# Optimization experiments

Hardware: AMD Instinct MI355X
Metric: run time of the kernel (lower is better)

## Reference

```python
import jax, jax.numpy as jnp
import numpy as np

B, L, D = 16, 1024, 256
H, FF = 8, 2048
DH = D // H
EPS = 1e-5


def setup_inputs() -> dict:
    key = jax.random.key(0)
    ks = jax.random.split(key, 13)
    s = 0.02
    return {
        "x": jax.random.normal(ks[0], (B, L, D), jnp.float32),
        "Wq": jax.random.normal(ks[1], (D, D), jnp.float32) * s,
        "bq": jnp.zeros((D,), jnp.float32),
        "Wk": jax.random.normal(ks[2], (D, D), jnp.float32) * s,
        "bk": jnp.zeros((D,), jnp.float32),
        "Wv": jax.random.normal(ks[3], (D, D), jnp.float32) * s,
        "bv": jnp.zeros((D,), jnp.float32),
        "Wo": jax.random.normal(ks[4], (D, D), jnp.float32) * s,
        "bo": jnp.zeros((D,), jnp.float32),
        "W1": jax.random.normal(ks[5], (D, FF), jnp.float32) * s,
        "b1": jnp.zeros((FF,), jnp.float32),
        "W2": jax.random.normal(ks[6], (FF, D), jnp.float32) * s,
        "b2": jnp.zeros((D,), jnp.float32),
        "g1": jnp.ones((D,), jnp.float32),
        "be1": jnp.zeros((D,), jnp.float32),
        "g2": jnp.ones((D,), jnp.float32),
        "be2": jnp.zeros((D,), jnp.float32),
    }


def _layernorm(x, g, b):
    m = jnp.mean(x, axis=-1, keepdims=True)
    v = jnp.mean(jnp.square(x - m), axis=-1, keepdims=True)
    return (x - m) * jax.lax.rsqrt(v + EPS) * g + b


def reference(x, Wq, bq, Wk, bk, Wv, bv, Wo, bo, W1, b1, W2, b2, g1, be1, g2, be2):
    b, l, d = x.shape
    # QKV projections, split heads (torch split/cat == reshape to [b,l,H,dh])
    q = (x @ Wq + bq).reshape(b, l, H, DH)
    k = (x @ Wk + bk).reshape(b, l, H, DH)
    v = (x @ Wv + bv).reshape(b, l, H, DH)
    # scaled dot-product attention per head
    scores = jnp.einsum("bqhd,bkhd->bhqk", q, k) / np.float32(DH) ** 0.5
    attn = jax.nn.softmax(scores, axis=-1)
    o = jnp.einsum("bhqk,bkhd->bqhd", attn, v).reshape(b, l, d)
    o = o @ Wo + bo
    # residual + LN1 (dropout p=0.0 -> identity)
    h = _layernorm(x + o, g1, be1)
    # FFN + residual + LN2
    ff = jax.nn.relu(h @ W1 + b1) @ W2 + b2
    return _layernorm(h + ff, g2, be2)
```

## Files before the change

kernel.cpp:

```cpp
#include <hip/hip_runtime.h>
#include <math.h>

#define B_  16
#define L_  1024
#define D_  256
#define H_  8
#define DH_ 32
#define FF_ 2048
#define NROW (B_*L_)
#define QKVS 768

typedef __attribute__((ext_vector_type(8))) short short8;
typedef __attribute__((ext_vector_type(4))) short short4v;
typedef __attribute__((ext_vector_type(4))) float f32x4;
typedef __attribute__((ext_vector_type(4))) unsigned uint4v;
typedef __attribute__((ext_vector_type(4))) unsigned short ushort4v;
typedef unsigned short ushortT;

__device__ inline ushortT f2bf(float f) {
    unsigned u = __builtin_bit_cast(unsigned, f);
    u += 0x7fffu + ((u >> 16) & 1u);
    return (ushortT)(u >> 16);
}

__device__ inline float bf2f(ushortT u) {
    return __builtin_bit_cast(float, (unsigned)u << 16);
}

__device__ inline float fexp2(float x) {
#if __has_builtin(__builtin_amdgcn_exp2f)
    return __builtin_amdgcn_exp2f(x);
#else
    return exp2f(x);
#endif
}

__device__ inline void gload_lds16(const ushortT* g, ushortT* l) {
    __builtin_amdgcn_global_load_lds(
        (const __attribute__((address_space(1))) unsigned*)g,
        (__attribute__((address_space(3))) unsigned*)l, 16, 0, 0);
}

__device__ inline unsigned lds_addr(const void* p) {
    return (unsigned)(size_t)(const __attribute__((address_space(3))) void*)p;
}

template<bool RELU, bool OBF16>
__global__ __launch_bounds__(256)
void gemm_bf16_kernel(const ushortT* __restrict__ A, const ushortT* __restrict__ Bt,
                      const float* __restrict__ bias, void* __restrict__ Cv,
                      int K, int ldb, int ldc)
{
    __shared__ ushortT As[2][128 * 32];
    __shared__ ushortT Bs[2][128 * 32];

    const int tid   = threadIdx.x;
    const int w     = tid >> 6;
    const int lane  = tid & 63;
    const int qlane = lane & 15;
    const int g     = lane >> 4;
    const int wm    = w >> 1, wn = w & 1;
    const int m0    = (blockIdx.x & 127) * 128;
    const int n0    = (blockIdx.x >> 7) * 128;

    int srowA[2], sq[2];
    #pragma unroll
    for (int j = 0; j < 2; ++j) {
        int idx = (j * 4 + w) * 64 + lane;
        srowA[j] = idx >> 2;
        sq[j]    = idx & 3;
    }

    f32x4 acc[4][4];
    #pragma unroll
    for (int mi = 0; mi < 4; ++mi)
        #pragma unroll
        for (int ni = 0; ni < 4; ++ni)
            acc[mi][ni] = (f32x4){0.f, 0.f, 0.f, 0.f};

    auto stage = [&](int buf, int kt) {
        const int k0 = kt * 32;
        #pragma unroll
        for (int j = 0; j < 2; ++j) {
            gload_lds16(A + (size_t)(m0 + srowA[j]) * K + k0 + sq[j] * 8,
                        &As[buf][(j * 4 + w) * 512]);
            gload_lds16(Bt + (size_t)(n0 + srowA[j]) * ldb + k0 + sq[j] * 8,
                        &Bs[buf][(j * 4 + w) * 512]);
        }
    };

    stage(0, 0);
    __syncthreads();

    const int nt = K >> 5;
    for (int t = 0; t < nt; ++t) {
        const int cur = t & 1;
        if (t + 1 < nt) stage(cur ^ 1, t + 1);

        short8 af[4], bfr[4];
        #pragma unroll
        for (int mi = 0; mi < 4; ++mi)
            af[mi] = *(const short8*)&As[cur][(wm * 64 + mi * 16 + qlane) * 32 + g * 8];
        #pragma unroll
        for (int ni = 0; ni < 4; ++ni)
            bfr[ni] = *(const short8*)&Bs[cur][(wn * 64 + ni * 16 + qlane) * 32 + g * 8];

        #pragma unroll
        for (int mi = 0; mi < 4; ++mi)
            #pragma unroll
            for (int ni = 0; ni < 4; ++ni)
                acc[mi][ni] = __builtin_amdgcn_mfma_f32_16x16x32_bf16(
                    af[mi], bfr[ni], acc[mi][ni], 0, 0, 0);

        __syncthreads();
    }

    #pragma unroll
    for (int mi = 0; mi < 4; ++mi) {
        #pragma unroll
        for (int ni = 0; ni < 4; ++ni) {
            const int n = n0 + wn * 64 + ni * 16 + qlane;
            const float bval = bias ? bias[n] : 0.f;
            #pragma unroll
            for (int r = 0; r < 4; ++r) {
                const int m = m0 + wm * 64 + mi * 16 + 4 * g + r;
                float v = acc[mi][ni][r] + bval;
                if (RELU)  v = fmaxf(v, 0.f);
                if (OBF16) ((ushortT*)Cv)[(size_t)m * ldc + n] = f2bf(v);
                else       ((float*)Cv)[(size_t)m * ldc + n] = v;
            }
        }
    }
}

template<bool OBF16>
__global__ __launch_bounds__(256)
void gemm64_kernel(const ushortT* __restrict__ A, const ushortT* __restrict__ Bt,
                   const float* __restrict__ bias, void* __restrict__ Cv, int K)
{
    __shared__ ushortT As[2][64 * 32];
    __shared__ ushortT Bs[2][64 * 32];

    const int tid   = threadIdx.x;
    const int w     = tid >> 6;
    const int lane  = tid & 63;
    const int qlane = lane & 15;
    const int g     = lane >> 4;
    const int bid   = blockIdx.x;
    const int m0    = (bid & 255) * 64;
    const int n0    = (bid >> 8) * 64;

    const int srow = tid >> 2;
    const int sq   = tid & 3;

    f32x4 acc[4];
    #pragma unroll
    for (int ni = 0; ni < 4; ++ni) acc[ni] = (f32x4){0.f, 0.f, 0.f, 0.f};

    auto stage = [&](int buf, int kt) {
        const int k0 = kt * 32;
        gload_lds16(A + (size_t)(m0 + srow) * K + k0 + sq * 8, &As[buf][w * 512]);
        gload_lds16(Bt + (size_t)(n0 + srow) * K + k0 + sq * 8, &Bs[buf][w * 512]);
    };

    stage(0, 0);
    __syncthreads();

    const int nt = K >> 5;
    for (int t = 0; t < nt; ++t) {
        const int cur = t & 1;
        if (t + 1 < nt) stage(cur ^ 1, t + 1);

        short8 af = *(const short8*)&As[cur][(w * 16 + qlane) * 32 + g * 8];
        short8 bfr[4];
        #pragma unroll
        for (int ni = 0; ni < 4; ++ni)
            bfr[ni] = *(const short8*)&Bs[cur][(ni * 16 + qlane) * 32 + g * 8];

        #pragma unroll
        for (int ni = 0; ni < 4; ++ni)
            acc[ni] = __builtin_amdgcn_mfma_f32_16x16x32_bf16(af, bfr[ni], acc[ni], 0, 0, 0);

        __syncthreads();
    }

    #pragma unroll
    for (int ni = 0; ni < 4; ++ni) {
        const int n = n0 + ni * 16 + qlane;
        const float bval = bias[n];
        #pragma unroll
        for (int r = 0; r < 4; ++r) {
            const int m = m0 + w * 16 + 4 * g + r;
            float v = acc[ni][r] + bval;
            if (OBF16) ((ushortT*)Cv)[(size_t)m * D_ + n] = f2bf(v);
            else       ((float*)Cv)[(size_t)m * D_ + n] = v;
        }
    }
}

template<bool XF32, bool YF32, bool OBF16>
__global__ __launch_bounds__(256)
void ln_kernel(const void* __restrict__ X, const void* __restrict__ Y,
               const float* __restrict__ g, const float* __restrict__ bb,
               void* __restrict__ out)
{
    const int tid  = threadIdx.x;
    const int lane = tid & 63;
    const int w    = tid >> 6;
    const size_t row = (size_t)blockIdx.x * 4 + w;
    const int c    = lane * 4;

    float xv[4], yv[4];
    if (XF32) {
        float4 v = *reinterpret_cast<const float4*>((const float*)X + row * D_ + c);
        xv[0] = v.x; xv[1] = v.y; xv[2] = v.z; xv[3] = v.w;
    } else {
        ushort4v v = *reinterpret_cast<const ushort4v*>((const ushortT*)X + row * D_ + c);
        #pragma unroll
        for (int j = 0; j < 4; ++j) xv[j] = bf2f(v[j]);
    }
    if (YF32) {
        float4 v = *reinterpret_cast<const float4*>((const float*)Y + row * D_ + c);
        yv[0] = v.x; yv[1] = v.y; yv[2] = v.z; yv[3] = v.w;
    } else {
        ushort4v v = *reinterpret_cast<const ushort4v*>((const ushortT*)Y + row * D_ + c);
        #pragma unroll
        for (int j = 0; j < 4; ++j) yv[j] = bf2f(v[j]);
    }

    float s0 = xv[0] + yv[0], s1 = xv[1] + yv[1], s2 = xv[2] + yv[2], s3 = xv[3] + yv[3];

    float sum = s0 + s1 + s2 + s3;
    float sq  = s0 * s0 + s1 * s1 + s2 * s2 + s3 * s3;
    #pragma unroll
    for (int off = 1; off < 64; off <<= 1) {
        sum += __shfl_xor(sum, off);
        sq  += __shfl_xor(sq, off);
    }
    const float mean = sum * (1.f / D_);
    const float var  = sq * (1.f / D_) - mean * mean;
    const float rinv = rsqrtf(var + 1e-5f);

    const float4 gv = *reinterpret_cast<const float4*>(g + c);
    const float4 bv = *reinterpret_cast<const float4*>(bb + c);
    float o0 = (s0 - mean) * rinv * gv.x + bv.x;
    float o1 = (s1 - mean) * rinv * gv.y + bv.y;
    float o2 = (s2 - mean) * rinv * gv.z + bv.z;
    float o3 = (s3 - mean) * rinv * gv.w + bv.w;

    if (OBF16) {
        unsigned p0 = (unsigned)f2bf(o0) | ((unsigned)f2bf(o1) << 16);
        unsigned p1 = (unsigned)f2bf(o2) | ((unsigned)f2bf(o3) << 16);
        uint2 u = {p0, p1};
        *reinterpret_cast<uint2*>((ushortT*)out + row * D_ + c) = u;
    } else {
        float4 ov = {o0, o1, o2, o3};
        *reinterpret_cast<float4*>((float*)out + row * D_ + c) = ov;
    }
}

__global__ __launch_bounds__(512)
void attn_mfma_kernel(const ushortT* __restrict__ qkv, ushortT* __restrict__ o)
{
    __shared__ __align__(16) ushortT K4[2][2048];
    __shared__ __align__(16) ushortT Vs[2][2048];

    const int tid   = threadIdx.x;
    const int lane  = tid & 63;
    const int w     = tid >> 6;
    const int qlane = lane & 15;
    const int g     = lane >> 4;

    const int bid = blockIdx.x;
    const int bh  = bid & 127;
    const int b   = bh >> 3;
    const int h   = bh & 7;
    const int q0  = (bid >> 7) * 128;

    const size_t inbase = (size_t)b * L_ * QKVS + h * 32;
    const size_t obase  = (size_t)b * L_ * 256 + h * 32;

    const short8 qf = *(const short8*)(qkv + inbase + (size_t)(q0 + w * 16 + qlane) * QKVS + g * 8);

    f32x4 ot0 = {0.f, 0.f, 0.f, 0.f}, ot1 = {0.f, 0.f, 0.f, 0.f};
    float l_reg = 0.f;

    const float CEXP = 0.25503540f;

    const int t2   = tid & 255;
    const int skey = t2 >> 2;
    const int sg   = t2 & 3;
    const bool isK = tid < 256;
    const ushortT* src = qkv + inbase + (isK ? 256 : 512) + sg * 8 + (size_t)skey * QKVS;

    char* K4b = (char*)&K4[0][0];
    char* Vsb = (char*)&Vs[0][0];

    unsigned kwoff = (unsigned)sg * 1024u + (unsigned)skey * 16u;
    kwoff ^= (kwoff >> 5) & 0x60;
    const unsigned vwoff = ((unsigned)((skey >> 2) * 2 + (sg >> 1))) * 128u +
                           ((unsigned)(skey & 3)) * 32u +
                           ((((unsigned)(sg & 1)) ^ ((unsigned)(sg >> 1))) * 16u);
    char* wbase = isK ? K4b : Vsb;
    const unsigned woff = isK ? kwoff : vwoff;

    unsigned kroff[4];
    #pragma unroll
    for (int kt4 = 0; kt4 < 4; ++kt4) {
        unsigned off = (unsigned)g * 1024u + (unsigned)(kt4 * 16 + qlane) * 16u;
        kroff[kt4] = off ^ ((off >> 5) & 0x60);
    }
    const unsigned vrbase  = lds_addr(&Vs[0][0]) + 256u * (unsigned)g + 8u * (unsigned)qlane;
    const unsigned vrbase2 = vrbase ^ 64u;

    short8 reg = *(const short8*)src;

    #pragma unroll 2
    for (int t = 0; t < L_ / 64; ++t) {
        const unsigned bo = (unsigned)(t & 1) * 4096u;
        *(short8*)(wbase + bo + woff) = reg;
        if (t + 1 < L_ / 64)
            reg = *(const short8*)(src + (size_t)((t + 1) * 64) * QKVS);
        __syncthreads();

        f32x4 st[4];
        __builtin_amdgcn_s_setprio(1);
        #pragma unroll
        for (int kt4 = 0; kt4 < 4; ++kt4) {
            short8 kf = *(const short8*)(K4b + bo + kroff[kt4]);
            st[kt4] = __builtin_amdgcn_mfma_f32_16x16x32_bf16(kf, qf, (f32x4){0.f,0.f,0.f,0.f}, 0, 0, 0);
        }
        __builtin_amdgcn_s_setprio(0);

        float p[16];
        float s4[4];
        #pragma unroll
        for (int kt4 = 0; kt4 < 4; ++kt4) {
            #pragma unroll
            for (int r = 0; r < 4; ++r)
                p[kt4 * 4 + r] = fexp2(st[kt4][r] * CEXP);
            s4[kt4] = (p[kt4*4] + p[kt4*4+1]) + (p[kt4*4+2] + p[kt4*4+3]);
        }
        float ssum = (s4[0] + s4[1]) + (s4[2] + s4[3]);
        ssum += __shfl_xor(ssum, 16);
        ssum += __shfl_xor(ssum, 32);
        l_reg += ssum;

        unsigned pk_[8];
        #pragma unroll
        for (int i = 0; i < 8; ++i)
            asm("v_cvt_pk_bf16_f32 %0, %1, %2" : "=v"(pk_[i]) : "v"(p[2*i]), "v"(p[2*i+1]));
        const short8 pa0 = __builtin_bit_cast(short8, (uint4v){pk_[0], pk_[1], pk_[2], pk_[3]});
        const short8 pa1 = __builtin_bit_cast(short8, (uint4v){pk_[4], pk_[5], pk_[6], pk_[7]});

        const unsigned va  = vrbase  + bo;
        const unsigned va2 = vrbase2 + bo;
        __builtin_amdgcn_s_setprio(1);
        {
            short4v v00, v01, v10, v11;
            asm volatile("ds_read_b64_tr_b16 %0, %1"             : "=v"(v00) : "v"(va));
            asm volatile("ds_read_b64_tr_b16 %0, %1 offset:1024" : "=v"(v01) : "v"(va));
            asm volatile("ds_read_b64_tr_b16 %0, %1 offset:128"  : "=v"(v10) : "v"(va2));
            asm volatile("ds_read_b64_tr_b16 %0, %1 offset:1152" : "=v"(v11) : "v"(va2));
            asm volatile("s_waitcnt lgkmcnt(0)" ::: "memory");
            __builtin_amdgcn_sched_barrier(0);
            short8 vb0 = __builtin_shufflevector(v00, v01, 0,1,2,3,4,5,6,7);
            short8 vb1 = __builtin_shufflevector(v10, v11, 0,1,2,3,4,5,6,7);
            ot0 = __builtin_amdgcn_mfma_f32_16x16x32_bf16(pa0, vb0, ot0, 0, 0, 0);
            ot1 = __builtin_amdgcn_mfma_f32_16x16x32_bf16(pa0, vb1, ot1, 0, 0, 0);
        }
        {
            short4v v00, v01, v10, v11;
            asm volatile("ds_read_b64_tr_b16 %0, %1 offset:2048" : "=v"(v00) : "v"(va));
            asm volatile("ds_read_b64_tr_b16 %0, %1 offset:3072" : "=v"(v01) : "v"(va));
            asm volatile("ds_read_b64_tr_b16 %0, %1 offset:2176" : "=v"(v10) : "v"(va2));
            asm volatile("ds_read_b64_tr_b16 %0, %1 offset:3200" : "=v"(v11) : "v"(va2));
            asm volatile("s_waitcnt lgkmcnt(0)" ::: "memory");
            __builtin_amdgcn_sched_barrier(0);
            short8 vb0 = __builtin_shufflevector(v00, v01, 0,1,2,3,4,5,6,7);
            short8 vb1 = __builtin_shufflevector(v10, v11, 0,1,2,3,4,5,6,7);
            ot0 = __builtin_amdgcn_mfma_f32_16x16x32_bf16(pa1, vb0, ot0, 0, 0, 0);
            ot1 = __builtin_amdgcn_mfma_f32_16x16x32_bf16(pa1, vb1, ot1, 0, 0, 0);
        }
        __builtin_amdgcn_s_setprio(0);
    }

    const float linv = 1.f / l_reg;
    #pragma unroll
    for (int r = 0; r < 4; ++r) {
        float lr = __shfl(linv, 4 * g + r);
        size_t row = (size_t)(q0 + w * 16 + 4 * g + r);
        ushortT* op = o + obase + row * 256;
        op[qlane]      = f2bf(ot0[r] * lr);
        op[16 + qlane] = f2bf(ot1[r] * lr);
    }
}

__global__ __launch_bounds__(256)
void prep_kernel(const float* __restrict__ x, ushortT* __restrict__ xb,
                 const float* __restrict__ Wq, const float* __restrict__ Wk,
                 const float* __restrict__ Wv, const float* __restrict__ Wo,
                 ushortT* __restrict__ Wqkvb, ushortT* __restrict__ Wob,
                 const float* __restrict__ W1, ushortT* __restrict__ W1b,
                 const float* __restrict__ W2, ushortT* __restrict__ W2b,
                 const float* __restrict__ bq, const float* __restrict__ bk,
                 const float* __restrict__ bv, float* __restrict__ bqkv)
{
    __shared__ float t[32][33];
    const int bid = blockIdx.x;
    const int tid = threadIdx.x;

    if (bid < 4096) {
        const int i = (bid * 256 + tid) * 4;
        float4 v = *reinterpret_cast<const float4*>(x + i);
        unsigned p0 = (unsigned)f2bf(v.x) | ((unsigned)f2bf(v.y) << 16);
        unsigned p1 = (unsigned)f2bf(v.z) | ((unsigned)f2bf(v.w) << 16);
        uint2 u = {p0, p1};
        *reinterpret_cast<uint2*>(xb + i) = u;
        return;
    }
    int i = bid - 4096;
    const float* W; ushortT* Wt; int K, N, bx, by;
    if (i < 256) {
        const int which = i >> 6, j = i & 63;
        bx = j & 7; by = j >> 3; K = 256; N = 256;
        W  = which == 0 ? Wq : which == 1 ? Wk : which == 2 ? Wv : Wo;
        Wt = which == 0 ? Wqkvb : which == 1 ? Wqkvb + 65536
           : which == 2 ? Wqkvb + 131072 : Wob;
    } else if (i < 768) {
        const int j = i - 256; bx = j & 63; by = j >> 6; K = 256; N = 2048;
        W = W1; Wt = W1b;
    } else if (i < 1280) {
        const int j = i - 768; bx = j & 7; by = j >> 3; K = 2048; N = 256;
        W = W2; Wt = W2b;
    } else {
        for (int k = tid; k < 768; k += 256)
            bqkv[k] = k < 256 ? bq[k] : (k < 512 ? bk[k - 256] : bv[k - 512]);
        return;
    }
    const int tx = tid & 31, ty = tid >> 5;
    const int k0 = by * 32, n0 = bx * 32;
    #pragma unroll
    for (int r = ty; r < 32; r += 8) t[r][tx] = W[(size_t)(k0 + r) * N + n0 + tx];
    __syncthreads();
    #pragma unroll
    for (int r = ty; r < 32; r += 8) Wt[(size_t)(n0 + r) * K + k0 + tx] = f2bf(t[tx][r]);
}

extern "C" void kernel_launch(void* const* d_in, const int* in_sizes, int n_in,
                              void* d_out, int out_size, void* d_ws, size_t ws_size,
                              hipStream_t stream)
{
    const float* x   = (const float*)d_in[0];
    const float* Wq  = (const float*)d_in[1];
    const float* bq  = (const float*)d_in[2];
    const float* Wk  = (const float*)d_in[3];
    const float* bk  = (const float*)d_in[4];
    const float* Wv  = (const float*)d_in[5];
    const float* bv  = (const float*)d_in[6];
    const float* Wo  = (const float*)d_in[7];
    const float* bo  = (const float*)d_in[8];
    const float* W1  = (const float*)d_in[9];
    const float* b1  = (const float*)d_in[10];
    const float* W2  = (const float*)d_in[11];
    const float* b2  = (const float*)d_in[12];
    const float* g1  = (const float*)d_in[13];
    const float* be1 = (const float*)d_in[14];
    const float* g2  = (const float*)d_in[15];
    const float* be2 = (const float*)d_in[16];
    float* out = (float*)d_out;

    char* wsb = (char*)d_ws;
    const size_t MB = (size_t)1 << 20;
    ushortT* Wqkvb = (ushortT*)(wsb);
    ushortT* Wob   = (ushortT*)(wsb + 393216);
    ushortT* W1b   = (ushortT*)(wsb + 512 * 1024);
    ushortT* W2b   = (ushortT*)(wsb + 1536 * 1024);
    float*   bqkv  = (float*)  (wsb + 2560 * 1024);
    ushortT* xb  = (ushortT*)(wsb + 3 * MB);
    ushortT* qkv = (ushortT*)(wsb + 11 * MB);
    ushortT* ob  = (ushortT*)(wsb + 35 * MB);
    ushortT* ao  = (ushortT*)(wsb + 43 * MB);
    ushortT* hb  = (ushortT*)(wsb + 3 * MB);
    ushortT* f1  = (ushortT*)(wsb + 11 * MB);

    prep_kernel<<<dim3(5377), dim3(256), 0, stream>>>(
        x, xb, Wq, Wk, Wv, Wo, Wqkvb, Wob, W1, W1b, W2, W2b, bq, bk, bv, bqkv);

    gemm_bf16_kernel<false, true><<<dim3(768), dim3(256), 0, stream>>>(
        xb, Wqkvb, bqkv, qkv, 256, 256, QKVS);

    attn_mfma_kernel<<<dim3(1024), dim3(512), 0, stream>>>(qkv, ob);

    gemm64_kernel<true><<<dim3(1024), dim3(256), 0, stream>>>(ob, Wob, bo, ao, 256);

    ln_kernel<false, false, true><<<dim3(NROW / 4), dim3(256), 0, stream>>>(
        xb, ao, g1, be1, hb);

    gemm_bf16_kernel<true, true><<<dim3(2048), dim3(256), 0, stream>>>(
        hb, W1b, b1, f1, 256, 256, FF_);

    gemm64_kernel<false><<<dim3(1024), dim3(256), 0, stream>>>(f1, W2b, b2, out, 2048);

    ln_kernel<false, true, false><<<dim3(NROW / 4), dim3(256), 0, stream>>>(
        hb, out, g2, be2, out);
}
```

Before: 145.3 us.

## Swizzle GEMM LDS tiles, deepen K-step to 64, unroll attention by two tiles

Applies an XOR swizzle to the LDS layout of both GEMM kernels to avoid bank conflicts. The 64x64 GEMM now stages K in steps of 64 instead of 32, which halves the number of barriers, and it gains RELU and ldc parameters so it can replace the 128x128 kernel for the W1 FFN GEMM (8192 blocks). The attention kernel loads two 64-key tiles per barrier using larger double buffers. The trade-offs are more LDS per block and smaller tiles for the FFN1 GEMM, which lowers operand reuse.

```diff
diff --git a/kernel.cpp b/kernel.cpp
--- a/kernel.cpp
+++ b/kernel.cpp
@@ -68,8 +68,9 @@
     for (int j = 0; j < 2; ++j) {
         int idx = (j * 4 + w) * 64 + lane;
         srowA[j] = idx >> 2;
-        sq[j]    = idx & 3;
-    }
+        sq[j]    = (idx & 3) ^ (srowA[j] & 3);
+    }
+    const int rsw = (g ^ (qlane & 3)) * 8;
 
     f32x4 acc[4][4];
     #pragma unroll
@@ -100,10 +101,10 @@
         short8 af[4], bfr[4];
         #pragma unroll
         for (int mi = 0; mi < 4; ++mi)
-            af[mi] = *(const short8*)&As[cur][(wm * 64 + mi * 16 + qlane) * 32 + g * 8];
+            af[mi] = *(const short8*)&As[cur][(wm * 64 + mi * 16 + qlane) * 32 + rsw];
         #pragma unroll
         for (int ni = 0; ni < 4; ++ni)
-            bfr[ni] = *(const short8*)&Bs[cur][(wn * 64 + ni * 16 + qlane) * 32 + g * 8];
+            bfr[ni] = *(const short8*)&Bs[cur][(wn * 64 + ni * 16 + qlane) * 32 + rsw];
 
         #pragma unroll
         for (int mi = 0; mi < 4; ++mi)
@@ -133,13 +134,14 @@
     }
 }
 
-template<bool OBF16>
+template<bool RELU, bool OBF16>
 __global__ __launch_bounds__(256)
 void gemm64_kernel(const ushortT* __restrict__ A, const ushortT* __restrict__ Bt,
-                   const float* __restrict__ bias, void* __restrict__ Cv, int K)
+                   const float* __restrict__ bias, void* __restrict__ Cv,
+                   int K, int ldc)
 {
-    __shared__ ushortT As[2][64 * 32];
-    __shared__ ushortT Bs[2][64 * 32];
+    __shared__ ushortT As[2][64 * 64];
+    __shared__ ushortT Bs[2][64 * 64];
 
     const int tid   = threadIdx.x;
     const int w     = tid >> 6;
@@ -150,36 +152,50 @@
     const int m0    = (bid & 255) * 64;
     const int n0    = (bid >> 8) * 64;
 
-    const int srow = tid >> 2;
-    const int sq   = tid & 3;
+    int srow[2], sq[2];
+    #pragma unroll
+    for (int j = 0; j < 2; ++j) {
+        const int c = j * 256 + tid;
+        srow[j] = c >> 3;
+        sq[j]   = (c & 7) ^ (srow[j] & 7);
+    }
 
     f32x4 acc[4];
     #pragma unroll
     for (int ni = 0; ni < 4; ++ni) acc[ni] = (f32x4){0.f, 0.f, 0.f, 0.f};
 
     auto stage = [&](int buf, int kt) {
-        const int k0 = kt * 32;
-        gload_lds16(A + (size_t)(m0 + srow) * K + k0 + sq * 8, &As[buf][w * 512]);
-        gload_lds16(Bt + (size_t)(n0 + srow) * K + k0 + sq * 8, &Bs[buf][w * 512]);
+        const int k0 = kt * 64;
+        #pragma unroll
+        for (int j = 0; j < 2; ++j) {
+            gload_lds16(A + (size_t)(m0 + srow[j]) * K + k0 + sq[j] * 8,
+                        &As[buf][(j * 256 + tid) * 8]);
+            gload_lds16(Bt + (size_t)(n0 + srow[j]) * K + k0 + sq[j] * 8,
+                        &Bs[buf][(j * 256 + tid) * 8]);
+        }
     };
 
     stage(0, 0);
     __syncthreads();
 
-    const int nt = K >> 5;
+    const int arow = w * 16 + qlane;
+    const int nt = K >> 6;
     for (int t = 0; t < nt; ++t) {
         const int cur = t & 1;
         if (t + 1 < nt) stage(cur ^ 1, t + 1);
 
-        short8 af = *(const short8*)&As[cur][(w * 16 + qlane) * 32 + g * 8];
-        short8 bfr[4];
-        #pragma unroll
-        for (int ni = 0; ni < 4; ++ni)
-            bfr[ni] = *(const short8*)&Bs[cur][(ni * 16 + qlane) * 32 + g * 8];
-
-        #pragma unroll
-        for (int ni = 0; ni < 4; ++ni)
-            acc[ni] = __builtin_amdgcn_mfma_f32_16x16x32_bf16(af, bfr[ni], acc[ni], 0, 0, 0);
+        #pragma unroll
+        for (int ks = 0; ks < 2; ++ks) {
+            const int aq = (ks * 4 + g) ^ (arow & 7);
+            short8 af = *(const short8*)&As[cur][arow * 64 + aq * 8];
+            #pragma unroll
+            for (int ni = 0; ni < 4; ++ni) {
+                const int brow = ni * 16 + qlane;
+                const int bq = (ks * 4 + g) ^ (brow & 7);
+                short8 bfr = *(const short8*)&Bs[cur][brow * 64 + bq * 8];
+                acc[ni] = __builtin_amdgcn_mfma_f32_16x16x32_bf16(af, bfr, acc[ni], 0, 0, 0);
+            }
+        }
 
         __syncthreads();
     }
@@ -192,8 +208,9 @@
         for (int r = 0; r < 4; ++r) {
             const int m = m0 + w * 16 + 4 * g + r;
             float v = acc[ni][r] + bval;
-            if (OBF16) ((ushortT*)Cv)[(size_t)m * D_ + n] = f2bf(v);
-            else       ((float*)Cv)[(size_t)m * D_ + n] = v;
+            if (RELU)  v = fmaxf(v, 0.f);
+            if (OBF16) ((ushortT*)Cv)[(size_t)m * ldc + n] = f2bf(v);
+            else       ((float*)Cv)[(size_t)m * ldc + n] = v;
         }
     }
 }
@@ -262,8 +279,8 @@
 __global__ __launch_bounds__(512)
 void attn_mfma_kernel(const ushortT* __restrict__ qkv, ushortT* __restrict__ o)
 {
-    __shared__ __align__(16) ushortT K4[2][2048];
-    __shared__ __align__(16) ushortT Vs[2][2048];
+    __shared__ __align__(16) ushortT K4[2][2][2048];
+    __shared__ __align__(16) ushortT Vs[2][2][2048];
 
     const int tid   = threadIdx.x;
     const int lane  = tid & 63;
@@ -293,8 +310,8 @@
     const bool isK = tid < 256;
     const ushortT* src = qkv + inbase + (isK ? 256 : 512) + sg * 8 + (size_t)skey * QKVS;
 
-    char* K4b = (char*)&K4[0][0];
-    char* Vsb = (char*)&Vs[0][0];
+    char* K4b = (char*)&K4[0][0][0];
+    char* Vsb = (char*)&Vs[0][0][0];
 
     unsigned kwoff = (unsigned)sg * 1024u + (unsigned)skey * 16u;
     kwoff ^= (kwoff >> 5) & 0x60;
@@ -310,79 +327,88 @@
         unsigned off = (unsigned)g * 1024u + (unsigned)(kt4 * 16 + qlane) * 16u;
         kroff[kt4] = off ^ ((off >> 5) & 0x60);
     }
-    const unsigned vrbase  = lds_addr(&Vs[0][0]) + 256u * (unsigned)g + 8u * (unsigned)qlane;
+    const unsigned vrbase  = lds_addr(&Vs[0][0][0]) + 256u * (unsigned)g + 8u * (unsigned)qlane;
     const unsigned vrbase2 = vrbase ^ 64u;
 
-    short8 reg = *(const short8*)src;
-
-    #pragma unroll 2
-    for (int t = 0; t < L_ / 64; ++t) {
-        const unsigned bo = (unsigned)(t & 1) * 4096u;
-        *(short8*)(wbase + bo + woff) = reg;
-        if (t + 1 < L_ / 64)
-            reg = *(const short8*)(src + (size_t)((t + 1) * 64) * QKVS);
+    short8 reg0 = *(const short8*)src;
+    short8 reg1 = *(const short8*)(src + (size_t)64 * QKVS);
+
+    for (int t = 0; t < L_ / 128; ++t) {
+        const unsigned bo = (unsigned)(t & 1) * 8192u;
+        *(short8*)(wbase + bo + woff)         = reg0;
+        *(short8*)(wbase + bo + 4096u + woff) = reg1;
+        if (t + 1 < L_ / 128) {
+            const size_t roff = (size_t)((t + 1) * 128) * QKVS;
+            reg0 = *(const short8*)(src + roff);
+            reg1 = *(const short8*)(src + roff + (size_t)64 * QKVS);
+        }
         __syncthreads();
 
-        f32x4 st[4];
-        __builtin_amdgcn_s_setprio(1);
-        #pragma unroll
-        for (int kt4 = 0; kt4 < 4; ++kt4) {
-            short8 kf = *(const short8*)(K4b + bo + kroff[kt4]);
-            st[kt4] = __builtin_amdgcn_mfma_f32_16x16x32_bf16(kf, qf, (f32x4){0.f,0.f,0.f,0.f}, 0, 0, 0);
-        }
-        __builtin_amdgcn_s_setprio(0);
-
-        float p[16];
-        float s4[4];
-        #pragma unroll
-        for (int kt4 = 0; kt4 < 4; ++kt4) {
+        #pragma unroll
+        for (int sub = 0; sub < 2; ++sub) {
+            const unsigned so = bo + (unsigned)sub * 4096u;
+
+            f32x4 st[4];
+            __builtin_amdgcn_s_setprio(1);
             #pragma unroll
-            for (int r = 0; r < 4; ++r)
-                p[kt4 * 4 + r] = fexp2(st[kt4][r] * CEXP);
-            s4[kt4] = (p[kt4*4] + p[kt4*4+1]) + (p[kt4*4+2] + p[kt4*4+3]);
-        }
-        float ssum = (s4[0] + s4[1]) + (s4[2] + s4[3]);
-        ssum += __shfl_xor(ssum, 16);
-        ssum += __shfl_xor(ssum, 32);
-        l_reg += ssum;
-
-        unsigned pk_[8];
-        #pragma unroll
-        for (int i = 0; i < 8; ++i)
-            asm("v_cvt_pk_bf16_f32 %0, %1, %2" : "=v"(pk_[i]) : "v"(p[2*i]), "v"(p[2*i+1]));
-        const short8 pa0 = __builtin_bit_cast(short8, (uint4v){pk_[0], pk_[1], pk_[2], pk_[3]});
-        const short8 pa1 = __builtin_bit_cast(short8, (uint4v){pk_[4], pk_[5], pk_[6], pk_[7]});
-
-        const unsigned va  = vrbase  + bo;
-        const unsigned va2 = vrbase2 + bo;
-        __builtin_amdgcn_s_setprio(1);
-        {
-            short4v v00, v01, v10, v11;
-            asm volatile("ds_read_b64_tr_b16 %0, %1"             : "=v"(v00) : "v"(va));
-            asm volatile("ds_read_b64_tr_b16 %0, %1 offset:1024" : "=v"(v01) : "v"(va));
-            asm volatile("ds_read_b64_tr_b16 %0, %1 offset:128"  : "=v"(v10) : "v"(va2));
-            asm volatile("ds_read_b64_tr_b16 %0, %1 offset:1152" : "=v"(v11) : "v"(va2));
-            asm volatile("s_waitcnt lgkmcnt(0)" ::: "memory");
-            __builtin_amdgcn_sched_barrier(0);
-            short8 vb0 = __builtin_shufflevector(v00, v01, 0,1,2,3,4,5,6,7);
-            short8 vb1 = __builtin_shufflevector(v10, v11, 0,1,2,3,4,5,6,7);
-            ot0 = __builtin_amdgcn_mfma_f32_16x16x32_bf16(pa0, vb0, ot0, 0, 0, 0);
-            ot1 = __builtin_amdgcn_mfma_f32_16x16x32_bf16(pa0, vb1, ot1, 0, 0, 0);
-        }
-        {
-            short4v v00, v01, v10, v11;
-            asm volatile("ds_read_b64_tr_b16 %0, %1 offset:2048" : "=v"(v00) : "v"(va));
-            asm volatile("ds_read_b64_tr_b16 %0, %1 offset:3072" : "=v"(v01) : "v"(va));
-            asm volatile("ds_read_b64_tr_b16 %0, %1 offset:2176" : "=v"(v10) : "v"(va2));
-            asm volatile("ds_read_b64_tr_b16 %0, %1 offset:3200" : "=v"(v11) : "v"(va2));
-            asm volatile("s_waitcnt lgkmcnt(0)" ::: "memory");
-            __builtin_amdgcn_sched_barrier(0);
-            short8 vb0 = __builtin_shufflevector(v00, v01, 0,1,2,3,4,5,6,7);
-            short8 vb1 = __builtin_shufflevector(v10, v11, 0,1,2,3,4,5,6,7);
-            ot0 = __builtin_amdgcn_mfma_f32_16x16x32_bf16(pa1, vb0, ot0, 0, 0, 0);
-            ot1 = __builtin_amdgcn_mfma_f32_16x16x32_bf16(pa1, vb1, ot1, 0, 0, 0);
-        }
-        __builtin_amdgcn_s_setprio(0);
+            for (int kt4 = 0; kt4 < 4; ++kt4) {
+                short8 kf = *(const short8*)(K4b + so + kroff[kt4]);
+                st[kt4] = __builtin_amdgcn_mfma_f32_16x16x32_bf16(kf, qf, (f32x4){0.f,0.f,0.f,0.f}, 0, 0, 0);
+            }
+            __builtin_amdgcn_s_setprio(0);
+
+            float p[16];
+            float s4[4];
+            #pragma unroll
+            for (int kt4 = 0; kt4 < 4; ++kt4) {
+                #pragma unroll
+                for (int r = 0; r < 4; ++r)
+                    p[kt4 * 4 + r] = fexp2(st[kt4][r] * CEXP);
+                s4[kt4] = (p[kt4*4] + p[kt4*4+1]) + (p[kt4*4+2] + p[kt4*4+3]);
+            }
+            float ssum = (s4[0] + s4[1]) + (s4[2] + s4[3]);
+            ssum += __shfl_xor(ssum, 16);
+            ssum += __shfl_xor(ssum, 32);
+            l_reg += ssum;
+
+            unsigned pk_[8];
+            #pragma unroll
+            for (int i = 0; i < 8; ++i)
+                asm("v_cvt_pk_bf16_f32 %0, %1, %2" : "=v"(pk_[i]) : "v"(p[2*i]), "v"(p[2*i+1]));
+            const short8 pa0 = __builtin_bit_cast(short8, (uint4v){pk_[0], pk_[1], pk_[2], pk_[3]});
+            const short8 pa1 = __builtin_bit_cast(short8, (uint4v){pk_[4], pk_[5], pk_[6], pk_[7]});
+
+            const unsigned va  = vrbase  + so;
+            const unsigned va2 = vrbase2 + so;
+            __builtin_amdgcn_s_setprio(1);
+            {
+                short4v v00, v01, v10, v11;
+                asm volatile("ds_read_b64_tr_b16 %0, %1"             : "=v"(v00) : "v"(va));
+                asm volatile("ds_read_b64_tr_b16 %0, %1 offset:1024" : "=v"(v01) : "v"(va));
+                asm volatile("ds_read_b64_tr_b16 %0, %1 offset:128"  : "=v"(v10) : "v"(va2));
+                asm volatile("ds_read_b64_tr_b16 %0, %1 offset:1152" : "=v"(v11) : "v"(va2));
+                asm volatile("s_waitcnt lgkmcnt(0)" ::: "memory");
+                __builtin_amdgcn_sched_barrier(0);
+                short8 vb0 = __builtin_shufflevector(v00, v01, 0,1,2,3,4,5,6,7);
+                short8 vb1 = __builtin_shufflevector(v10, v11, 0,1,2,3,4,5,6,7);
+                ot0 = __builtin_amdgcn_mfma_f32_16x16x32_bf16(pa0, vb0, ot0, 0, 0, 0);
+                ot1 = __builtin_amdgcn_mfma_f32_16x16x32_bf16(pa0, vb1, ot1, 0, 0, 0);
+            }
+            {
+                short4v v00, v01, v10, v11;
+                asm volatile("ds_read_b64_tr_b16 %0, %1 offset:2048" : "=v"(v00) : "v"(va));
+                asm volatile("ds_read_b64_tr_b16 %0, %1 offset:3072" : "=v"(v01) : "v"(va));
+                asm volatile("ds_read_b64_tr_b16 %0, %1 offset:2176" : "=v"(v10) : "v"(va2));
+                asm volatile("ds_read_b64_tr_b16 %0, %1 offset:3200" : "=v"(v11) : "v"(va2));
+                asm volatile("s_waitcnt lgkmcnt(0)" ::: "memory");
+                __builtin_amdgcn_sched_barrier(0);
+                short8 vb0 = __builtin_shufflevector(v00, v01, 0,1,2,3,4,5,6,7);
+                short8 vb1 = __builtin_shufflevector(v10, v11, 0,1,2,3,4,5,6,7);
+                ot0 = __builtin_amdgcn_mfma_f32_16x16x32_bf16(pa1, vb0, ot0, 0, 0, 0);
+                ot1 = __builtin_amdgcn_mfma_f32_16x16x32_bf16(pa1, vb1, ot1, 0, 0, 0);
+            }
+            __builtin_amdgcn_s_setprio(0);
+        }
     }
 
     const float linv = 1.f / l_reg;
@@ -492,15 +518,17 @@
 
     attn_mfma_kernel<<<dim3(1024), dim3(512), 0, stream>>>(qkv, ob);
 
-    gemm64_kernel<true><<<dim3(1024), dim3(256), 0, stream>>>(ob, Wob, bo, ao, 256);
+    gemm64_kernel<false, true><<<dim3(1024), dim3(256), 0, stream>>>(
+        ob, Wob, bo, ao, 256, 256);
 
     ln_kernel<false, false, true><<<dim3(NROW / 4), dim3(256), 0, stream>>>(
         xb, ao, g1, be1, hb);
 
-    gemm_bf16_kernel<true, true><<<dim3(2048), dim3(256), 0, stream>>>(
-        hb, W1b, b1, f1, 256, 256, FF_);
-
-    gemm64_kernel<false><<<dim3(1024), dim3(256), 0, stream>>>(f1, W2b, b2, out, 2048);
+    gemm64_kernel<true, true><<<dim3(8192), dim3(256), 0, stream>>>(
+        hb, W1b, b1, f1, 256, FF_);
+
+    gemm64_kernel<false, false><<<dim3(1024), dim3(256), 0, stream>>>(
+        f1, W2b, b2, out, 2048, 256);
 
     ln_kernel<false, true, false><<<dim3(NROW / 4), dim3(256), 0, stream>>>(
         hb, out, g2, be2, out);
```

After: 137.9 us. 5.1% less time.
